# Performance work log

Hardware: AMD Instinct MI355X
Metric: run time of the kernel (lower is better)

The kernel has to match this reference:

```python
import jax, jax.numpy as jnp
import numpy as np
import math

B, S, D, H = 4, 2048, 1024, 16
HD = D // H
EPS = 1e-10


def setup_inputs() -> dict:
    key = jax.random.key(0)
    kx, kq, kk, kv, ko = jax.random.split(key, 5)
    x = jax.random.normal(kx, (B, S, D), dtype=jnp.float32)
    # causal additive mask: 0 on/below diagonal, -1e9 above
    mask = jnp.where(jnp.triu(jnp.ones((S, S), dtype=bool), k=1), -1e9, 0.0).astype(jnp.float32)
    scale = 1.0 / math.sqrt(D)
    Wq = jax.random.normal(kq, (D, D), dtype=jnp.float32) * scale
    Wk = jax.random.normal(kk, (D, D), dtype=jnp.float32) * scale
    Wv = jax.random.normal(kv, (D, D), dtype=jnp.float32) * scale
    Wo = jax.random.normal(ko, (D, D), dtype=jnp.float32) * scale
    return {"x": x, "mask": mask, "Wq": Wq, "Wk": Wk, "Wv": Wv, "Wo": Wo}


def _nirmalya_softmax(t):
    # faithful to original: plain exp (no max-subtraction), eps in denominator
    p1 = jnp.exp(t)
    return p1 / (jnp.sum(p1, axis=-1, keepdims=True) + EPS)


def reference(x, mask, Wq, Wk, Wv, Wo):
    b, s, d = x.shape
    # torch Linear (bias=False): y = x @ W.T
    def proj(W):
        y = jnp.einsum('bsd,ed->bse', x, W)
        return y.reshape(b, s, H, HD).transpose(0, 2, 1, 3)  # [b,h,s,hd]
    q, k, v = proj(Wq), proj(Wk), proj(Wv)
    scores = jnp.einsum('bhqd,bhkd->bhqk', q, k) / math.sqrt(HD)
    scores = scores + mask  # broadcast over batch/heads
    attn = _nirmalya_softmax(scores)
    out = jnp.einsum('bhqk,bhkd->bhqd', attn, v)
    out = out.transpose(0, 2, 1, 3).reshape(b, s, d)
    return jnp.einsum('bsd,ed->bse', out, Wo)
```

## Files before the change

### kernel.cpp

```cpp
#include <hip/hip_runtime.h>
#include <hip/hip_bf16.h>

typedef __bf16 bf16;
typedef __attribute__((ext_vector_type(8))) __bf16 bf16x8;
typedef __attribute__((ext_vector_type(4))) float f32x4;

#define MFMA16(a, b, c) __builtin_amdgcn_mfma_f32_16x16x32_bf16((a), (b), (c), 0, 0, 0)

#define GLOAD_LDS16(gp, lp)                                                              \
  __builtin_amdgcn_global_load_lds(                                                      \
      (const __attribute__((address_space(1))) unsigned int*)(gp),                       \
      (__attribute__((address_space(3))) unsigned int*)(lp), 16, 0, 0)

#define BAR()   __builtin_amdgcn_s_barrier()
#define LGKM0() asm volatile("s_waitcnt lgkmcnt(0)" ::: "memory")
#define VMC(n)  asm volatile("s_waitcnt vmcnt(" #n ")" ::: "memory")
#define PRIO1() __builtin_amdgcn_s_setprio(1)
#define PRIO0() __builtin_amdgcn_s_setprio(0)

__global__ __launch_bounds__(256) void cvt_all(const float* __restrict__ x,
                                               const float* __restrict__ wq,
                                               const float* __restrict__ wk,
                                               const float* __restrict__ wv,
                                               const float* __restrict__ wo,
                                               bf16* __restrict__ xb,
                                               bf16* __restrict__ wqkv,
                                               bf16* __restrict__ wob) {
  constexpr int NXC = 8388608 / 8;
  constexpr int NWC = 1048576 / 8;
  constexpr int TOT = NXC + 4 * NWC;
  for (int c = blockIdx.x * 256 + threadIdx.x; c < TOT; c += gridDim.x * 256) {
    const float* src; bf16* dst; int idx;
    if (c < NXC) { src = x; dst = xb; idx = c; }
    else {
      int c2 = c - NXC; int wsel = c2 >> 17; idx = c2 & (NWC - 1);
      src = wsel == 0 ? wq : wsel == 1 ? wk : wsel == 2 ? wv : wo;
      dst = wsel < 3 ? wqkv + (size_t)wsel * 1048576 : wob;
    }
    float4 v0 = reinterpret_cast<const float4*>(src)[idx * 2];
    float4 v1 = reinterpret_cast<const float4*>(src)[idx * 2 + 1];
    bf16x8 o;
    o[0] = (bf16)v0.x; o[1] = (bf16)v0.y; o[2] = (bf16)v0.z; o[3] = (bf16)v0.w;
    o[4] = (bf16)v1.x; o[5] = (bf16)v1.y; o[6] = (bf16)v1.z; o[7] = (bf16)v1.w;
    reinterpret_cast<bf16x8*>(dst)[idx] = o;
  }
}

#define MMA8(BF, MH, NH)                                                                 \
  _Pragma("unroll") for (int mi = 0; mi < 2; ++mi)                                       \
  _Pragma("unroll") for (int ni = 0; ni < 2; ++ni)                                       \
  _Pragma("unroll") for (int ks = 0; ks < 2; ++ks)                                       \
      acc[(MH) * 2 + mi][(NH) * 2 + ni] =                                                \
          MFMA16(af[mi][ks], (BF)[ni][ks], acc[(MH) * 2 + mi][(NH) * 2 + ni]);

template <int MODE, int NT>
__global__ __launch_bounds__(512, 1) void gemm8(const bf16* __restrict__ A,
                                                const bf16* __restrict__ B,
                                                void* __restrict__ Cv,
                                                bf16* __restrict__ VT) {
  constexpr int K = 1024;
  __shared__ bf16 smem[49152];
  const int tid = threadIdx.x, lane = tid & 63, w = tid >> 6;
  const int l15 = lane & 15, l16 = lane >> 4;
  const int wr = w >> 2, wc = w & 3;
  const int lin = blockIdx.x;
  const int idx = lin >> 3;
  const int mt = (lin & 7) * 8 + idx / NT;
  const int nt = idx % NT;
  const int bm0 = mt * 128, bn0 = nt * 256;

  auto stA = [&](int buf, int t, int j) {
    const int r = j * 64 + (tid >> 3);
    const int g = (tid & 7) ^ (r & 7);
    GLOAD_LDS16(&A[(size_t)(bm0 + r) * K + t * 64 + g * 8],
                &smem[buf * 8192 + j * 4096 + tid * 8]);
  };
  auto stB = [&](int buf, int t, int j) {
    const int r = j * 64 + (tid >> 3);
    const int g = (tid & 7) ^ (r & 7);
    GLOAD_LDS16(&B[(size_t)(bn0 + r) * K + t * 64 + g * 8],
                &smem[16384 + buf * 16384 + j * 4096 + tid * 8]);
  };
  bf16x8 af[2][2], b0[2][2], b1[2][2];
  auto ldA = [&](int buf, int mh, bf16x8 (&dst)[2][2]) {
#pragma unroll
    for (int mi = 0; mi < 2; ++mi)
#pragma unroll
      for (int ks = 0; ks < 2; ++ks)
        dst[mi][ks] = *reinterpret_cast<const bf16x8*>(
            &smem[buf * 8192 + (wr * 64 + mh * 32 + mi * 16 + l15) * 64 +
                  (((ks * 4 + l16) ^ (l15 & 7)) * 8)]);
  };
  auto ldB = [&](int buf, int nh, bf16x8 (&dst)[2][2]) {
#pragma unroll
    for (int ni = 0; ni < 2; ++ni)
#pragma unroll
      for (int ks = 0; ks < 2; ++ks)
        dst[ni][ks] = *reinterpret_cast<const bf16x8*>(
            &smem[16384 + buf * 16384 + (wc * 64 + nh * 32 + ni * 16 + l15) * 64 +
                  (((ks * 4 + l16) ^ (l15 & 7)) * 8)]);
  };

  f32x4 acc[4][4] = {};

  stA(0, 0, 0); stA(0, 0, 1);
  stB(0, 0, 0); stB(0, 0, 1); stB(0, 0, 2); stB(0, 0, 3);
  stA(1, 1, 0); stA(1, 1, 1);
  stB(1, 1, 0); stB(1, 1, 1); stB(1, 1, 2); stB(1, 1, 3);
  VMC(6); BAR();

#pragma unroll 1
  for (int it = 0; it < K / 128; ++it) {
    const int t0 = 2 * it;
    const bool last = (it == K / 128 - 1);
    ldA(0, 0, af); ldB(0, 0, b0);
    BAR(); LGKM0();
    PRIO1(); MMA8(b0, 0, 0); PRIO0();
    BAR();
    ldB(0, 1, b1);
    BAR(); LGKM0();
    PRIO1(); MMA8(b1, 0, 1); PRIO0();
    BAR();
    ldA(0, 1, af);
    BAR(); LGKM0();
    PRIO1(); MMA8(b1, 1, 1); PRIO0();
    BAR();
    if (!last) {
      stA(0, t0 + 2, 0); stA(0, t0 + 2, 1);
      stB(0, t0 + 2, 0); stB(0, t0 + 2, 1); stB(0, t0 + 2, 2); stB(0, t0 + 2, 3);
    }
    PRIO1(); MMA8(b0, 1, 0); PRIO0();
    if (last) { VMC(0); } else { VMC(6); }
    BAR();
    ldA(1, 0, af); ldB(1, 0, b0);
    BAR(); LGKM0();
    PRIO1(); MMA8(b0, 0, 0); PRIO0();
    BAR();
    ldB(1, 1, b1);
    BAR(); LGKM0();
    PRIO1(); MMA8(b1, 0, 1); PRIO0();
    BAR();
    ldA(1, 1, af);
    BAR(); LGKM0();
    PRIO1(); MMA8(b1, 1, 1); PRIO0();
    BAR();
    if (!last) {
      stA(1, t0 + 3, 0); stA(1, t0 + 3, 1);
      stB(1, t0 + 3, 0); stB(1, t0 + 3, 1); stB(1, t0 + 3, 2); stB(1, t0 + 3, 3);
    }
    PRIO1(); MMA8(b0, 1, 0); PRIO0();
    if (!last) VMC(6);
    BAR();
  }

  if constexpr (MODE == 0) {
#pragma unroll
    for (int i = 0; i < 4; ++i)
#pragma unroll
      for (int j = 0; j < 4; ++j)
#pragma unroll
        for (int r = 0; r < 4; ++r) {
          const size_t row = bm0 + wr * 64 + (i >> 1) * 32 + (i & 1) * 16 + l16 * 4 + r;
          const size_t col = bn0 + wc * 64 + (j >> 1) * 32 + (j & 1) * 16 + l15;
          reinterpret_cast<float*>(Cv)[row * (NT * 256) + col] = acc[i][j][r];
        }
  } else {
    if (bn0 < 2048) {
#pragma unroll
      for (int i = 0; i < 4; ++i)
#pragma unroll
        for (int j = 0; j < 4; ++j)
#pragma unroll
          for (int r = 0; r < 4; ++r) {
            const size_t row = bm0 + wr * 64 + (i >> 1) * 32 + (i & 1) * 16 + l16 * 4 + r;
            const size_t col = bn0 + wc * 64 + (j >> 1) * 32 + (j & 1) * 16 + l15;
            reinterpret_cast<bf16*>(Cv)[row * 2048 + col] = (bf16)acc[i][j][r];
          }
    } else {
#pragma unroll
      for (int i = 0; i < 4; ++i)
#pragma unroll
        for (int j = 0; j < 4; ++j)
#pragma unroll
          for (int r = 0; r < 4; ++r) {
            const int m = wr * 64 + (i >> 1) * 32 + (i & 1) * 16 + l16 * 4 + r;
            const int n = wc * 64 + (j >> 1) * 32 + (j & 1) * 16 + l15;
            smem[n * 136 + m] = (bf16)acc[i][j][r];
          }
      BAR();
      const int n = tid >> 1, half = tid & 1;
      const size_t vbase = ((size_t)(bm0 >> 11) * 1024 + (bn0 - 2048 + n)) * 2048 +
                           (bm0 & 2047) + half * 64;
#pragma unroll
      for (int k = 0; k < 8; ++k) {
        bf16x8 v = *reinterpret_cast<const bf16x8*>(&smem[n * 136 + half * 64 + k * 8]);
        *reinterpret_cast<bf16x8*>(&VT[vbase + k * 8]) = v;
      }
    }
  }
}

constexpr int S_ = 2048, H_ = 16, LDQK = 2048;

__global__ __launch_bounds__(256) void attn_kernel(const bf16* __restrict__ QK,
                                                   const bf16* __restrict__ VT,
                                                   bf16* __restrict__ AO) {
  __shared__ bf16 Ks[2][64 * 64];
  __shared__ bf16 Vs[2][64 * 64];
  __shared__ bf16 Ps[4][32 * 64];
  const int tid = threadIdx.x, lane = tid & 63, w = tid >> 6;
  const int l15 = lane & 15, l16 = lane >> 4;
  const int bh = blockIdx.x, b = bh >> 4, h = bh & (H_ - 1);
  const int qy = blockIdx.y;
  const int qt = qy ^ (((qy >> 2) & 1) * 3);
  const int q0 = qt * 128;
  const size_t qoff = (size_t)b * S_ * LDQK + h * 64;
  const size_t koff = qoff + 1024;
  const size_t voff = (size_t)bh * 64 * LDQK;
  const int qrow = q0 + w * 32;
  const int tmax = (qrow + 31) >> 6;

  auto stage = [&](int t) {
    const int kv0 = t * 64, bs = t & 1;
#pragma unroll
    for (int i = 0; i < 2; ++i) {
      const int c = tid + 256 * i;
      const int row = c >> 3, gs = (c & 7) ^ (row & 7);
      GLOAD_LDS16(&QK[koff + (size_t)(kv0 + row) * LDQK + gs * 8], &Ks[bs][c * 8]);
      GLOAD_LDS16(&VT[voff + (size_t)row * LDQK + kv0 + gs * 8], &Vs[bs][c * 8]);
    }
  };

  bf16x8 qf[2][2];
#pragma unroll
  for (int mi = 0; mi < 2; ++mi)
#pragma unroll
    for (int kk = 0; kk < 2; ++kk)
      qf[mi][kk] = *reinterpret_cast<const bf16x8*>(
          &QK[qoff + (size_t)(qrow + mi * 16 + l15) * LDQK + kk * 32 + l16 * 8]);

  f32x4 o[2][4] = {};
  float rs[2][4] = {};
  const int ntiles = 2 * qt + 2;

  stage(0);
  VMC(0); BAR();

  for (int t = 0; t < ntiles; ++t) {
    if (t + 1 < ntiles) stage(t + 1);
    if (t <= tmax) {
      const int bs = t & 1;
      const int kv0 = t * 64;
      f32x4 sc[2][4] = {};
      bf16x8 kf[4][2];
#pragma unroll
      for (int ni = 0; ni < 4; ++ni)
#pragma unroll
        for (int kk = 0; kk < 2; ++kk)
          kf[ni][kk] = *reinterpret_cast<bf16x8*>(
              &Ks[bs][(ni * 16 + l15) * 64 + (((kk * 4 + l16) ^ (l15 & 7)) * 8)]);
#pragma unroll
      for (int mi = 0; mi < 2; ++mi)
#pragma unroll
        for (int ni = 0; ni < 4; ++ni)
#pragma unroll
          for (int kk = 0; kk < 2; ++kk)
            sc[mi][ni] = MFMA16(qf[mi][kk], kf[ni][kk], sc[mi][ni]);

      if (t == tmax) {
#pragma unroll
        for (int mi = 0; mi < 2; ++mi)
#pragma unroll
          for (int ni = 0; ni < 4; ++ni)
#pragma unroll
            for (int r = 0; r < 4; ++r) {
              const int lrow = mi * 16 + l16 * 4 + r;
              const int lcol = ni * 16 + l15;
              float p = (kv0 + lcol <= qrow + lrow) ? __expf(sc[mi][ni][r] * 0.125f) : 0.0f;
              rs[mi][r] += p;
              Ps[w][lrow * 64 + (lcol ^ ((lrow & 7) << 3))] = (bf16)p;
            }
      } else {
#pragma unroll
        for (int mi = 0; mi < 2; ++mi)
#pragma unroll
          for (int ni = 0; ni < 4; ++ni)
#pragma unroll
            for (int r = 0; r < 4; ++r) {
              const int lrow = mi * 16 + l16 * 4 + r;
              const int lcol = ni * 16 + l15;
              float p = __expf(sc[mi][ni][r] * 0.125f);
              rs[mi][r] += p;
              Ps[w][lrow * 64 + (lcol ^ ((lrow & 7) << 3))] = (bf16)p;
            }
      }

      bf16x8 pf[2][2], vf[4][2];
#pragma unroll
      for (int mi = 0; mi < 2; ++mi)
#pragma unroll
        for (int kk = 0; kk < 2; ++kk)
          pf[mi][kk] = *reinterpret_cast<bf16x8*>(
              &Ps[w][(mi * 16 + l15) * 64 + (((kk * 4 + l16) ^ (l15 & 7)) * 8)]);
#pragma unroll
      for (int ni = 0; ni < 4; ++ni)
#pragma unroll
        for (int kk = 0; kk < 2; ++kk)
          vf[ni][kk] = *reinterpret_cast<bf16x8*>(
              &Vs[bs][(ni * 16 + l15) * 64 + (((kk * 4 + l16) ^ (l15 & 7)) * 8)]);
#pragma unroll
      for (int mi = 0; mi < 2; ++mi)
#pragma unroll
        for (int ni = 0; ni < 4; ++ni)
#pragma unroll
          for (int kk = 0; kk < 2; ++kk)
            o[mi][ni] = MFMA16(pf[mi][kk], vf[ni][kk], o[mi][ni]);
    }
    VMC(0); BAR();
  }

#pragma unroll
  for (int mi = 0; mi < 2; ++mi)
#pragma unroll
    for (int r = 0; r < 4; ++r) {
      float v = rs[mi][r];
      v += __shfl_xor(v, 1);
      v += __shfl_xor(v, 2);
      v += __shfl_xor(v, 4);
      v += __shfl_xor(v, 8);
      rs[mi][r] = v + 1e-10f;
    }

  const size_t aoff = (size_t)b * S_ * 1024 + h * 64;
#pragma unroll
  for (int mi = 0; mi < 2; ++mi)
#pragma unroll
    for (int ni = 0; ni < 4; ++ni)
#pragma unroll
      for (int r = 0; r < 4; ++r) {
        int row = qrow + mi * 16 + l16 * 4 + r;
        AO[aoff + (size_t)row * 1024 + ni * 16 + l15] = (bf16)(o[mi][ni][r] / rs[mi][r]);
      }
}

extern "C" void kernel_launch(void* const* d_in, const int* in_sizes, int n_in,
                              void* d_out, int out_size, void* d_ws, size_t ws_size,
                              hipStream_t stream) {
  const float* x  = (const float*)d_in[0];
  const float* Wq = (const float*)d_in[2];
  const float* Wk = (const float*)d_in[3];
  const float* Wv = (const float*)d_in[4];
  const float* Wo = (const float*)d_in[5];

  constexpr int B = 4, S = 2048, D = 1024;
  constexpr size_t nx = (size_t)B * S * D;
  constexpr size_t nw = (size_t)D * D;

  char* ws = (char*)d_ws;
  bf16* xb    = (bf16*)ws;
  bf16* Wqkvb = xb + nx;
  bf16* Wob   = Wqkvb + 3 * nw;
  bf16* QKb   = Wob + nw;
  bf16* VTb   = QKb + (size_t)B * S * 2048;
  bf16* AOb   = VTb + nx;

  cvt_all<<<2048, 256, 0, stream>>>(x, Wq, Wk, Wv, Wo, xb, Wqkvb, Wob);

  gemm8<2, 12><<<768, 512, 0, stream>>>(xb, Wqkvb, QKb, VTb);

  attn_kernel<<<dim3(B * H_, S / 128), 256, 0, stream>>>(QKb, VTb, AOb);

  gemm8<0, 4><<<256, 512, 0, stream>>>(AOb, Wob, d_out, nullptr);
}
```

Measured before the change: 182.5 us.

## Split P staging into two 32-column halves interleaved with PV MFMAs

```diff
diff --git a/kernel.cpp b/kernel.cpp
--- a/kernel.cpp
+++ b/kernel.cpp
@@ -207,7 +207,7 @@
                                                    bf16* __restrict__ AO) {
   __shared__ bf16 Ks[2][64 * 64];
   __shared__ bf16 Vs[2][64 * 64];
-  __shared__ bf16 Ps[4][32 * 64];
+  __shared__ bf16 PsH[4][32 * 32];
   const int tid = threadIdx.x, lane = tid & 63, w = tid >> 6;
   const int l15 = lane & 15, l16 = lane >> 4;
   const int bh = blockIdx.x, b = bh >> 4, h = bh & (H_ - 1);
@@ -242,6 +242,8 @@
   f32x4 o[2][4] = {};
   float rs[2][4] = {};
   const int ntiles = 2 * qt + 2;
+  const int psl = l16 * 128 + (l15 & 7);
+  const int Hx = (l15 >> 3) ^ l16;
 
   stage(0);
   VMC(0); BAR();
@@ -267,54 +269,43 @@
           for (int kk = 0; kk < 2; ++kk)
             sc[mi][ni] = MFMA16(qf[mi][kk], kf[ni][kk], sc[mi][ni]);
 
-      if (t == tmax) {
+      const bool diag = (t == tmax);
+#pragma unroll
+      for (int kb = 0; kb < 2; ++kb) {
 #pragma unroll
         for (int mi = 0; mi < 2; ++mi)
 #pragma unroll
+          for (int nih = 0; nih < 2; ++nih) {
+            const int ni = kb * 2 + nih;
+#pragma unroll
+            for (int r = 0; r < 4; ++r) {
+              float p = __expf(sc[mi][ni][r] * 0.125f);
+              if (diag) {
+                const int grow = qrow + mi * 16 + l16 * 4 + r;
+                const int gcol = kv0 + ni * 16 + l15;
+                p = (gcol <= grow) ? p : 0.0f;
+              }
+              rs[mi][r] += p;
+              PsH[w][mi * 512 + r * 32 + psl + ((((nih * 2) ^ r) ^ Hx) << 3)] = (bf16)p;
+            }
+          }
+        bf16x8 pf[2];
+#pragma unroll
+        for (int mi = 0; mi < 2; ++mi)
+          pf[mi] = *reinterpret_cast<bf16x8*>(
+              &PsH[w][(mi * 16 + l15) * 32 +
+                      ((l16 ^ (l15 & 3) ^ ((l15 >> 2) & 3)) << 3)]);
+        bf16x8 vf[4];
+#pragma unroll
+        for (int ni = 0; ni < 4; ++ni)
+          vf[ni] = *reinterpret_cast<bf16x8*>(
+              &Vs[bs][(ni * 16 + l15) * 64 + (((kb * 4 + l16) ^ (l15 & 7)) * 8)]);
+#pragma unroll
+        for (int mi = 0; mi < 2; ++mi)
+#pragma unroll
           for (int ni = 0; ni < 4; ++ni)
-#pragma unroll
-            for (int r = 0; r < 4; ++r) {
-              const int lrow = mi * 16 + l16 * 4 + r;
-              const int lcol = ni * 16 + l15;
-              float p = (kv0 + lcol <= qrow + lrow) ? __expf(sc[mi][ni][r] * 0.125f) : 0.0f;
-              rs[mi][r] += p;
-              Ps[w][lrow * 64 + (lcol ^ ((lrow & 7) << 3))] = (bf16)p;
-            }
-      } else {
-#pragma unroll
-        for (int mi = 0; mi < 2; ++mi)
-#pragma unroll
-          for (int ni = 0; ni < 4; ++ni)
-#pragma unroll
-            for (int r = 0; r < 4; ++r) {
-              const int lrow = mi * 16 + l16 * 4 + r;
-              const int lcol = ni * 16 + l15;
-              float p = __expf(sc[mi][ni][r] * 0.125f);
-              rs[mi][r] += p;
-              Ps[w][lrow * 64 + (lcol ^ ((lrow & 7) << 3))] = (bf16)p;
-            }
+            o[mi][ni] = MFMA16(pf[mi], vf[ni], o[mi][ni]);
       }
-
-      bf16x8 pf[2][2], vf[4][2];
-#pragma unroll
-      for (int mi = 0; mi < 2; ++mi)
-#pragma unroll
-        for (int kk = 0; kk < 2; ++kk)
-          pf[mi][kk] = *reinterpret_cast<bf16x8*>(
-              &Ps[w][(mi * 16 + l15) * 64 + (((kk * 4 + l16) ^ (l15 & 7)) * 8)]);
-#pragma unroll
-      for (int ni = 0; ni < 4; ++ni)
-#pragma unroll
-        for (int kk = 0; kk < 2; ++kk)
-          vf[ni][kk] = *reinterpret_cast<bf16x8*>(
-              &Vs[bs][(ni * 16 + l15) * 64 + (((kk * 4 + l16) ^ (l15 & 7)) * 8)]);
-#pragma unroll
-      for (int mi = 0; mi < 2; ++mi)
-#pragma unroll
-        for (int ni = 0; ni < 4; ++ni)
-#pragma unroll
-          for (int kk = 0; kk < 2; ++kk)
-            o[mi][ni] = MFMA16(pf[mi][kk], vf[ni][kk], o[mi][ni]);
     }
     VMC(0); BAR();
   }
```

New measurement: 191.1 us. 1.05x slower.
